# Performance work log

Measured on AMD Instinct MI355X. Metric: run time of the kernel, lower is better.

Reference implementation:

```python
import jax, jax.numpy as jnp
import numpy as np

B, S, V, D, G, H, L, K = 32, 256, 100000, 128, 128, 256, 32, 3
ALPHA = 0.5


def lstm_pass(x, mask, W, U, b, reverse):
    # x: (B,S,I), mask: (B,S) bool. PyTorch gate order i,f,g,o.
    Bh = x.shape[0]
    Hd = U.shape[0]
    h0 = jnp.zeros((Bh, Hd), x.dtype)
    c0 = jnp.zeros((Bh, Hd), x.dtype)

    def step(carry, inp):
        h, c = carry
        xt, mt = inp
        g = xt @ W + h @ U + b
        i, f, gg, o = jnp.split(g, 4, axis=-1)
        i = jax.nn.sigmoid(i)
        f = jax.nn.sigmoid(f)
        gg = jnp.tanh(gg)
        o = jax.nn.sigmoid(o)
        cn = f * c + i * gg
        hn = o * jnp.tanh(cn)
        m = mt[:, None]
        h = jnp.where(m, hn, h)
        c = jnp.where(m, cn, c)
        return (h, c), h * m.astype(h.dtype)

    _, hs = jax.lax.scan(step, (h0, c0), (x.transpose(1, 0, 2), mask.T), reverse=reverse)
    return hs.transpose(1, 0, 2)  # (B,S,Hd), zero at padded steps (like pad_packed)


def setup_inputs() -> dict:
    key = jax.random.key(0)
    ks = jax.random.split(key, 24)
    word_inputs = jax.random.randint(ks[0], (B, S), 0, V)
    lens = jnp.sort(jax.random.randint(ks[1], (B,), S // 2, S + 1))[::-1]
    mask = (jnp.arange(S)[None, :] < lens[:, None])
    idx_inputs = jax.random.randint(ks[2], (B, S), 0, V)
    char_inputs = jax.random.randint(ks[3], (B * S, 4), 0, 100)
    char_seq_lengths = jnp.ones((B * S,), jnp.int64 if jax.config.jax_enable_x64 else jnp.int32)
    char_seq_recover = jnp.arange(B * S)
    s = lambda k, sh, sc: jax.random.normal(k, sh, jnp.float32) * sc
    I = D + G
    inp = {
        'word_inputs': word_inputs,
        'word_seq_lengths': lens,
        'char_inputs': char_inputs,
        'char_seq_lengths': char_seq_lengths,
        'char_seq_recover': char_seq_recover,
        'mask': mask,
        'idx_inputs': idx_inputs,
        'word_embedding': s(ks[4], (V, D), 0.1),
        'label_embedding': s(ks[5], (L, D), 0.1),
        'sent_W': s(ks[6], (D, G), 1.0 / np.sqrt(D)),
        'sent_b': jnp.zeros((G,), jnp.float32),
        'conv_W': s(ks[7], (L, L, K), 1.0 / np.sqrt(L * K)),
        'conv_b': jnp.zeros((L,), jnp.float32),
        'lstm_Wf': s(ks[8], (I, 4 * H // 2), 1.0 / np.sqrt(I)),
        'lstm_Uf': s(ks[9], (H // 2, 4 * H // 2), 1.0 / np.sqrt(H // 2)),
        'lstm_bf': jnp.zeros((4 * H // 2,), jnp.float32),
        'lstm_Wb': s(ks[10], (I, 4 * H // 2), 1.0 / np.sqrt(I)),
        'lstm_Ub': s(ks[11], (H // 2, 4 * H // 2), 1.0 / np.sqrt(H // 2)),
        'lstm_bb': jnp.zeros((4 * H // 2,), jnp.float32),
        'tag_W': s(ks[12], (H, L), 1.0 / np.sqrt(H)),
        'tag_b': jnp.zeros((L,), jnp.float32),
        'mem_W': s(ks[13], (H, L), 1.0 / np.sqrt(H)),
        'mem_b': jnp.zeros((L,), jnp.float32),
        'mem_bank': s(ks[14], (V, H), 0.1),
    }
    return inp


def reference(word_inputs, word_seq_lengths, char_inputs, char_seq_lengths, char_seq_recover,
              mask, idx_inputs, word_embedding, label_embedding, sent_W, sent_b,
              conv_W, conv_b, lstm_Wf, lstm_Uf, lstm_bf, lstm_Wb, lstm_Ub, lstm_bb,
              tag_W, tag_b, mem_W, mem_b, mem_bank):
    maskf = mask.astype(jnp.float32)
    # ---- WordRep: embeddings + label cosine similarity ----
    we = word_embedding[word_inputs]  # (B,S,D) gather
    wn = we / (jnp.linalg.norm(we, axis=-1, keepdims=True) + 1e-8)
    ln = label_embedding / (jnp.linalg.norm(label_embedding, axis=-1, keepdims=True) + 1e-8)
    label_embs = jnp.einsum('bsd,ld->bsl', wn, ln)  # (B,S,L)
    # ---- SentenceRep (projection stand-in) + label attention pooling ----
    sent_hidden = jnp.tanh(we @ sent_W + sent_b)  # (B,S,G)
    lf = jax.lax.conv_general_dilated(
        label_embs.transpose(0, 2, 1), conv_W, (1,), [(K // 2, K // 2)],
        dimension_numbers=('NCH', 'OIH', 'NCH')) + conv_b[None, :, None]
    lf = jax.nn.relu(lf).transpose(0, 2, 1)  # (B,S,L)
    lm = lf.max(axis=-1)  # (B,S)
    # partial (masked) softmax, exactly as in the torch code
    e = jnp.exp(lm) * maskf
    attn = e / e.sum(axis=1, keepdims=True)
    sent_rep = jnp.einsum('bs,bsg->bg', attn, sent_hidden)[:, None, :]  # bmm
    sent_rep = jnp.broadcast_to(sent_rep, (B, S, G))  # repeat over seq
    # ---- BiLSTM over concat(word, sentence) ----
    wr = jnp.concatenate([we, sent_rep], axis=-1)  # (B,S,D+G)
    hf = lstm_pass(wr, mask, lstm_Wf, lstm_Uf, lstm_bf, False)
    hb = lstm_pass(wr, mask, lstm_Wb, lstm_Ub, lstm_bb, True)
    feat = jnp.concatenate([hf, hb], axis=-1)  # (B,S,H)
    outputs = feat @ tag_W + tag_b  # (B,S,L)
    # ---- MemoryBank: gather keyed by word id, zero padded positions ----
    doc_h = mem_bank[word_inputs] * maskf[..., None]  # (B,S,H) irregular gather
    doc_rep = doc_h @ mem_W + mem_b  # mem2tag
    # bank update (side effect in torch; computed functionally, not returned)
    new_bank = mem_bank.at[idx_inputs.reshape(-1)].set(
        (feat * maskf[..., None]).reshape(-1, H))
    del new_bank
    return outputs * (1.0 - ALPHA) + doc_rep * ALPHA
```

## Files before the change

kernel.cpp:

```cpp
#include <hip/hip_runtime.h>
#include <hip/hip_bf16.h>

#define BB 32
#define SS 256
#define DD 128
#define GG 128
#define NG 512
#define LL 32
#define LOG2E 1.4426950408889634f

typedef unsigned short u16;
typedef __attribute__((ext_vector_type(8))) short short8;
typedef __attribute__((ext_vector_type(4))) float f32x4;

__device__ __forceinline__ float bf2f(u16 u){ return __uint_as_float(((unsigned)u)<<16); }
__device__ __forceinline__ u16 f2bf(float f){
    unsigned x = __float_as_uint(f);
    unsigned r = x + 0x7fffu + ((x>>16)&1u);
    return (u16)(r>>16);
}
__device__ __forceinline__ float tanh_f(float x){ float e=__expf(2.0f*x); return 1.0f - 2.0f/(e+1.0f); }

__device__ __forceinline__ float exp2_f(float x){
#if __has_builtin(__builtin_amdgcn_exp2f)
    return __builtin_amdgcn_exp2f(x);
#elif __has_builtin(__builtin_amdgcn_expf)
    return __builtin_amdgcn_expf(x);
#else
    return __expf(x * 0.6931471805599453f);
#endif
}
__device__ __forceinline__ float rcp_f(float x){
#if __has_builtin(__builtin_amdgcn_rcpf)
    return __builtin_amdgcn_rcpf(x);
#else
    return 1.0f / x;
#endif
}

struct PJobs { const void* src[21]; int n[21]; int p0[21]; int p1[21]; int type[21]; };

__global__ void kprep(PJobs jb, const void* __restrict__ wemb, int* __restrict__ flags,
                      float* __restrict__ can,
                      u16* __restrict__ WcatT, u16* __restrict__ tagWT, u16* __restrict__ memWT){
    int t = threadIdx.x;
    __shared__ int cw[4];
    __shared__ int sflag;
    {
        u16 v = ((const u16*)wemb)[2*t];
        int e = (v>>7)&0xFF;
        int c = (e>=0x90)?1:0;
        #pragma unroll
        for (int mk=32; mk>0; mk>>=1) c += __shfl_xor(c, mk);
        if ((t&63)==0) cw[t>>6] = c;
        __syncthreads();
        if (t==0) sflag = (cw[0]+cw[1]+cw[2]+cw[3] >= 32) ? 1 : 0;
        __syncthreads();
    }
    int f = sflag;
    if (blockIdx.x==0 && blockIdx.y==0 && t==0) flags[0] = f;

    int id = blockIdx.y;
    int i = blockIdx.x*256 + t;
    if (i >= jb.n[id]) return;
    const void* src = jb.src[id];
    int p0 = jb.p0[id];
    int ty = jb.type[id];
    if (ty == 0){
        float v = f ? ((const float*)src)[i] : bf2f(((const u16*)src)[i]);
        can[p0 + i] = v;
    } else if (ty == 1){
        int c = i>>7, k = i&127;
        float v = f ? ((const float*)src)[k*jb.p1[id] + c] : bf2f(((const u16*)src)[k*jb.p1[id] + c]);
        WcatT[(size_t)(p0 + c)*128 + k] = f2bf(v);
    } else if (ty == 2){
        int l = i&31, k = i>>5;
        float v = f ? ((const float*)src)[k*32 + l] : bf2f(((const u16*)src)[k*32 + l]);
        (p0 ? memWT : tagWT)[l*256 + k] = f2bf(v);
    } else {
        int row = i>>7, col = i&127;
        float v = f ? ((const float*)src)[i] : bf2f(((const u16*)src)[i]);
        float sq = v*v;
        #pragma unroll
        for (int mk=32; mk>0; mk>>=1) sq += __shfl_xor(sq, mk);
        __shared__ float r4[4];
        if ((t&63)==0) r4[t>>6] = sq;
        __syncthreads();
        int half = t>>7;
        float tot = r4[half*2] + r4[half*2+1];
        float inv = 1.0f/(sqrtf(tot) + 1e-8f);
        WcatT[(size_t)(1152+row)*128 + col] = f2bf(v*inv);
        WcatT[(size_t)(1184+row)*128 + col] = 0;
    }
}

__global__ void k1_token(const int* __restrict__ wid, const void* __restrict__ wemb,
                         const int* __restrict__ flags,
                         u16* __restrict__ weC, float* __restrict__ invn){
    int blk = blockIdx.x;
    int t = threadIdx.x;
    int idx = wid[blk];
    float wv = flags[0] ? ((const float*)wemb)[(size_t)idx*DD + t]
                        : bf2f(((const u16*)wemb)[(size_t)idx*DD + t]);
    int b = blk>>8, s = blk&255;
    int m = s*BB + b;
    weC[(size_t)m*DD + t] = f2bf(wv);
    float sq = wv*wv;
    #pragma unroll
    for (int mk=32; mk>0; mk>>=1) sq += __shfl_xor(sq, mk);
    __shared__ float red2[2];
    if ((t&63)==0) red2[t>>6] = sq;
    __syncthreads();
    if (t==0) invn[m] = 1.0f/(sqrtf(red2[0]+red2[1]) + 1e-8f);
}

__global__ __launch_bounds__(256) void kgemm(const u16* __restrict__ weC,
                      const u16* __restrict__ WcatT,
                      const float* __restrict__ invn, const float* __restrict__ sentBc,
                      float* __restrict__ gpre4, float* __restrict__ sent_h,
                      float* __restrict__ lab_e){
    int mt = blockIdx.x;
    int nb = blockIdx.y;
    int t = threadIdx.x;
    int w4 = t>>6, l = t&63, li = l&15, lg = l>>4;
    int mbase = mt*64 + w4*16;
    int n0 = nb*64;
    short8 af[4];
    #pragma unroll
    for (int ks=0;ks<4;ks++)
        af[ks] = *(const short8*)&weC[(size_t)(mbase + li)*128 + ks*32 + lg*8];
    f32x4 acc[4];
    #pragma unroll
    for (int nt=0;nt<4;nt++){
        short8 bf[4];
        #pragma unroll
        for (int ks=0;ks<4;ks++)
            bf[ks] = *(const short8*)&WcatT[(size_t)(n0 + nt*16 + li)*128 + ks*32 + lg*8];
        f32x4 a; a[0]=0.f; a[1]=0.f; a[2]=0.f; a[3]=0.f;
        #pragma unroll
        for (int ks=0;ks<4;ks++)
            a = __builtin_amdgcn_mfma_f32_16x16x32_bf16(af[ks], bf[ks], a, 0,0,0);
        acc[nt] = a;
    }
    int mrow = mbase + lg*4;
    #pragma unroll
    for (int nt=0;nt<4;nt++){
        int n = n0 + nt*16 + li;
        if (n < 1024){
            int dir = n>>9, n2 = n&511;
            int q = n2>>7, cc = n2&127, w5 = cc>>4, li5 = cc&15;
            float sc = (q==2) ? 2.0f*LOG2E : LOG2E;
            #pragma unroll
            for (int r=0;r<4;r++){
                int m = mrow + r;
                int b = m&31, s = m>>5;
                int bg = b>>2, rb = b&3;
                gpre4[((size_t)((dir*8+bg)*256 + s)*8 + w5)*256 + (rb*16 + li5)*4 + q] = acc[nt][r]*sc;
            }
        } else if (n < 1152){
            int c = n - 1024;
            float bb = sentBc[c];
            #pragma unroll
            for (int r=0;r<4;r++){
                int m = mrow + r;
                int b = m&31, s = m>>5;
                sent_h[((size_t)(b*256+s))*128 + c] = tanh_f(acc[nt][r] + bb);
            }
        } else if (n < 1184){
            int c = n - 1152;
            #pragma unroll
            for (int r=0;r<4;r++){
                int m = mrow + r;
                int b = m&31, s = m>>5;
                lab_e[((size_t)(b*256+s))*32 + c] = acc[nt][r] * invn[m];
            }
        }
    }
}

__global__ __launch_bounds__(256) void k2_conv(const float* __restrict__ lab_e,
                        const float* __restrict__ convWc, const float* __restrict__ convBc,
                        const int* __restrict__ lens, float* __restrict__ e_ws){
    int b = blockIdx.x, stile = blockIdx.y, t = threadIdx.x;
    int sl = t>>3, oq = t&7;
    int s = stile*32 + sl;
    __shared__ float le_s[34*33];
    __shared__ float wle[LL*LL*3];
    __shared__ float wb[LL];
    int s0 = stile*32;
    for (int i=t; i<34*32; i+=256){
        int row = i>>5, col = i&31;
        int sg = s0 - 1 + row;
        le_s[row*33 + col] = (sg>=0 && sg<SS) ? lab_e[(size_t)b*SS*LL + sg*LL + col] : 0.f;
    }
    for (int i=t; i<LL*LL*3; i+=256) wle[i] = convWc[i];
    if (t < LL) wb[t] = convBc[t];
    __syncthreads();
    float lm = 0.f;
    #pragma unroll
    for (int op=0; op<4; op++){
        int o = oq*4 + op;
        float a0 = wb[o], a1 = 0.f, a2 = 0.f;
        #pragma unroll
        for (int i=0;i<LL;i++){
            a0 = fmaf(le_s[(sl+0)*33+i], wle[o*96 + i*3    ], a0);
            a1 = fmaf(le_s[(sl+1)*33+i], wle[o*96 + i*3 + 1], a1);
            a2 = fmaf(le_s[(sl+2)*33+i], wle[o*96 + i*3 + 2], a2);
        }
        lm = fmaxf(lm, fmaxf(a0+a1+a2, 0.f));
    }
    #pragma unroll
    for (int mk=1; mk<8; mk<<=1) lm = fmaxf(lm, __shfl_xor(lm, mk));
    if (oq == 0) e_ws[b*SS + s] = (s < lens[b]) ? __expf(lm) : 0.f;
}

__global__ void k3a_attn(const float* __restrict__ e_ws, const float* __restrict__ sent_h,
                         float* __restrict__ srp, float* __restrict__ esum_p){
    int b = blockIdx.x, st = blockIdx.y, t = threadIdx.x;
    int col = t&127, sh = t>>7;
    __shared__ float es[32];
    __shared__ float red[2][GG];
    if (t < 32) es[t] = e_ws[b*SS + st*32 + t];
    __syncthreads();
    int sb = st*32 + sh*16;
    float a0 = 0.f, a1 = 0.f;
    #pragma unroll
    for (int s2=0; s2<16; s2+=2){
        a0 = fmaf(es[sh*16+s2],   sent_h[((size_t)b*SS + sb+s2)*GG + col], a0);
        a1 = fmaf(es[sh*16+s2+1], sent_h[((size_t)b*SS + sb+s2+1)*GG + col], a1);
    }
    red[sh][col] = a0+a1;
    __syncthreads();
    if (t < GG) srp[((size_t)b*8 + st)*GG + t] = red[0][t] + red[1][t];
    if (t < 32){
        float e = es[t];
        #pragma unroll
        for (int mk=16; mk>0; mk>>=1) e += __shfl_xor(e, mk);
        if (t==0) esum_p[b*8 + st] = e;
    }
}

__global__ void k3b_cpart(const float* __restrict__ srp, const float* __restrict__ esum_p,
                          const float* __restrict__ Wfc, const float* __restrict__ Wbc,
                          const float* __restrict__ bfc, const float* __restrict__ bbc,
                          float* __restrict__ cpart){
    int chunk = blockIdx.x, b = blockIdx.y, t = threadIdx.x;
    __shared__ float srs[GG];
    if (t < GG){
        float a = 0.f;
        #pragma unroll
        for (int st=0; st<8; st++) a += srp[((size_t)b*8 + st)*GG + t];
        float es = 0.f;
        #pragma unroll
        for (int st=0; st<8; st++) es += esum_p[b*8 + st];
        srs[t] = a * (1.0f/es);
    }
    __syncthreads();
    int ng = chunk*256 + t;
    int dir = ng>>9, n = ng&511;
    const float* W = dir ? Wbc : Wfc;
    float c0 = (dir ? bbc : bfc)[n], c1 = 0.f;
    for (int g=0; g<GG; g+=2){
        c0 = fmaf(srs[g],   W[(size_t)(DD+g)*NG + n], c0);
        c1 = fmaf(srs[g+1], W[(size_t)(DD+g+1)*NG + n], c1);
    }
    cpart[((size_t)dir*NG + n)*BB + b] = c0+c1;
}

__global__ __launch_bounds__(512) void k5_lstm(const float* __restrict__ gpre4,
                       const float* __restrict__ Ufc, const float* __restrict__ Ubc,
                       const float* __restrict__ cpart,
                       const int* __restrict__ lens, float* __restrict__ feat){
    int dir = blockIdx.x>>3, bg = blockIdx.x&7;
    int t = threadIdx.x;
    int w = t>>6, l = t&63, lg = l>>4, li = l&15;
    int j = w*16 + li;
    int b = bg*4 + lg;
    const float* Uc = dir ? Ubc : Ufc;

    short8 bfr[4][4];
    #pragma unroll
    for (int q=0;q<4;q++){
        float sc = (q==2) ? 2.0f*LOG2E : LOG2E;
        #pragma unroll
        for (int ks=0;ks<4;ks++){
            int n = q*128 + j;
            short8 v;
            #pragma unroll
            for (int jj=0;jj<8;jj++)
                v[jj] = (short)f2bf(Uc[(size_t)(ks*32 + lg*8 + jj)*NG + n] * sc);
            bfr[q][ks] = v;
        }
    }
    float cpr[4];
    #pragma unroll
    for (int q=0;q<4;q++)
        cpr[q] = cpart[((size_t)(dir*NG + q*128 + j))*BB + b] * ((q==2) ? 2.0f*LOG2E : LOG2E);
    int len1 = lens[b];

    __shared__ u16 Hhi[2][16*128];
    for (int i=t; i<2*2048; i+=512) ((u16*)Hhi)[i] = 0;

    bool rdp = ((li & 3) == 0);
    int roff[4];
    #pragma unroll
    for (int ks=0;ks<4;ks++)
        roff[ks] = (li*256 + ((ks*64 + lg*16) ^ ((li&7)<<4))) >> 1;
    int woff;
    { int row = lg*4; woff = (row*256 + ((2*j) ^ ((row&7)<<4))) >> 1; }

    short8 ah[4];
    #pragma unroll
    for (int ks=0;ks<4;ks++){
        #pragma unroll
        for (int jj=0;jj<8;jj++) ah[ks][jj] = 0;
    }

    float c = 0.f, h = 0.f;
    int sgn = dir ? -1 : 1;
    int s0 = dir ? (SS-1) : 0;
    const float* gl = gpre4 + ((size_t)(dir*8 + bg)*256 + s0)*2048 + w*256 + l*4;
    ptrdiff_t gstep = (ptrdiff_t)sgn * 2048;

    f32x4 gA = *(const f32x4*)gl;
    f32x4 gB = *(const f32x4*)(gl + gstep);
    const float* glp = gl + 2*gstep;

    float* fb = feat + ((size_t)b*SS + s0)*256 + dir*128 + j;
    ptrdiff_t fstep = (ptrdiff_t)sgn * 256;

    int s = s0;
    __syncthreads();

#define K5_STEP(P, G)                                                          \
    {                                                                          \
        if (rdp){                                                              \
            ah[0] = *(const short8*)&Hhi[P][roff[0]];                          \
            ah[1] = *(const short8*)&Hhi[P][roff[1]];                          \
            ah[2] = *(const short8*)&Hhi[P][roff[2]];                          \
            ah[3] = *(const short8*)&Hhi[P][roff[3]];                          \
        }                                                                      \
        f32x4 ac[4];                                                           \
        _Pragma("unroll")                                                      \
        for (int q=0;q<4;q++){ f32x4 z; z[0]=G[q]+cpr[q]; z[1]=0.f; z[2]=0.f; z[3]=0.f; ac[q]=z; } \
        if (tt2 + 2 < SS){ G = *(const f32x4*)glp; glp += gstep; }             \
        _Pragma("unroll")                                                      \
        for (int ks=0;ks<4;ks++){                                              \
            _Pragma("unroll")                                                  \
            for (int q=0;q<4;q++)                                              \
                ac[q] = __builtin_amdgcn_mfma_f32_16x16x32_bf16(ah[ks], bfr[q][ks], ac[q], 0,0,0); \
        }                                                                      \
        float si = rcp_f(1.0f + exp2_f(-ac[0][0]));                            \
        float sf = rcp_f(1.0f + exp2_f(-ac[1][0]));                            \
        float tg = 1.0f - 2.0f*rcp_f(exp2_f(ac[2][0]) + 1.0f);                 \
        float so = rcp_f(1.0f + exp2_f(-ac[3][0]));                            \
        float cn = sf*c + si*tg;                                               \
        float th = 1.0f - 2.0f*rcp_f(exp2_f(cn*(2.0f*LOG2E)) + 1.0f);          \
        float hn = so*th;                                                      \
        if (s < 128){ c = cn; h = hn; fb[0] = hn; }                            \
        else { bool mm = (s < len1); c = mm?cn:c; h = mm?hn:h; fb[0] = mm?hn:0.f; } \
        Hhi[P^1][woff] = f2bf(h);                                              \
        asm volatile("s_waitcnt lgkmcnt(0)" ::: "memory");                     \
        __builtin_amdgcn_sched_barrier(0);                                     \
        __builtin_amdgcn_s_barrier();                                          \
        __builtin_amdgcn_sched_barrier(0);                                     \
        s += sgn; fb += fstep;                                                 \
    }

    for (int tt=0; tt<SS; tt+=2){
        { int tt2 = tt;   K5_STEP(0, gA) }
        { int tt2 = tt+1; K5_STEP(1, gB) }
    }
#undef K5_STEP
}

__global__ void k6_final(const float* __restrict__ feat, const int* __restrict__ wid,
                         const int* __restrict__ lens,
                         const u16* __restrict__ tagWT, const float* __restrict__ tagBc,
                         const u16* __restrict__ memWT, const float* __restrict__ memBc,
                         const void* __restrict__ bank, const int* __restrict__ flags,
                         void* __restrict__ out){
    int t = threadIdx.x;
    int tok = blockIdx.x*8 + (t>>5);
    int lcol = t&31;
    int b = tok>>8, s = tok&255;
    int f32m = flags[0];
    int idx = wid[tok];
    bool m = s < lens[b];
    const float* fr = feat + (size_t)tok*256;
    float a0 = tagBc[lcol], a1=0.f, a2=0.f, a3=0.f;
    #pragma unroll 4
    for (int cc=0; cc<32; cc++){
        short8 tw = *(const short8*)&tagWT[lcol*256 + cc*8];
        a0 = fmaf(fr[cc*8+0], bf2f((u16)tw[0]), a0);
        a1 = fmaf(fr[cc*8+1], bf2f((u16)tw[1]), a1);
        a2 = fmaf(fr[cc*8+2], bf2f((u16)tw[2]), a2);
        a3 = fmaf(fr[cc*8+3], bf2f((u16)tw[3]), a3);
        a0 = fmaf(fr[cc*8+4], bf2f((u16)tw[4]), a0);
        a1 = fmaf(fr[cc*8+5], bf2f((u16)tw[5]), a1);
        a2 = fmaf(fr[cc*8+6], bf2f((u16)tw[6]), a2);
        a3 = fmaf(fr[cc*8+7], bf2f((u16)tw[7]), a3);
    }
    float r1 = (a0+a1)+(a2+a3);
    float b0 = memBc[lcol], b1=0.f, b2=0.f, b3=0.f;
    if (m){
        if (f32m){
            const float* br = (const float*)bank + (size_t)idx*256;
            #pragma unroll 4
            for (int cc=0; cc<32; cc++){
                short8 tw = *(const short8*)&memWT[lcol*256 + cc*8];
                b0 = fmaf(br[cc*8+0], bf2f((u16)tw[0]), b0);
                b1 = fmaf(br[cc*8+1], bf2f((u16)tw[1]), b1);
                b2 = fmaf(br[cc*8+2], bf2f((u16)tw[2]), b2);
                b3 = fmaf(br[cc*8+3], bf2f((u16)tw[3]), b3);
                b0 = fmaf(br[cc*8+4], bf2f((u16)tw[4]), b0);
                b1 = fmaf(br[cc*8+5], bf2f((u16)tw[5]), b1);
                b2 = fmaf(br[cc*8+6], bf2f((u16)tw[6]), b2);
                b3 = fmaf(br[cc*8+7], bf2f((u16)tw[7]), b3);
            }
        } else {
            const u16* br = (const u16*)bank + (size_t)idx*256;
            #pragma unroll 4
            for (int cc=0; cc<32; cc++){
                short8 tw = *(const short8*)&memWT[lcol*256 + cc*8];
                short8 bv = *(const short8*)&br[cc*8];
                b0 = fmaf(bf2f((u16)bv[0]), bf2f((u16)tw[0]), b0);
                b1 = fmaf(bf2f((u16)bv[1]), bf2f((u16)tw[1]), b1);
                b2 = fmaf(bf2f((u16)bv[2]), bf2f((u16)tw[2]), b2);
                b3 = fmaf(bf2f((u16)bv[3]), bf2f((u16)tw[3]), b3);
                b0 = fmaf(bf2f((u16)bv[4]), bf2f((u16)tw[4]), b0);
                b1 = fmaf(bf2f((u16)bv[5]), bf2f((u16)tw[5]), b1);
                b2 = fmaf(bf2f((u16)bv[6]), bf2f((u16)tw[6]), b2);
                b3 = fmaf(bf2f((u16)bv[7]), bf2f((u16)tw[7]), b3);
            }
        }
    }
    float r2 = (b0+b1)+(b2+b3);
    float res = 0.5f*r1 + 0.5f*r2;
    if (f32m) ((float*)out)[(size_t)tok*LL + lcol] = res;
    else      ((u16*)out)[(size_t)tok*LL + lcol]   = f2bf(res);
}

extern "C" void kernel_launch(void* const* d_in, const int* in_sizes, int n_in,
                              void* d_out, int out_size, void* d_ws, size_t ws_size,
                              hipStream_t stream){
    const int* wid  = (const int*)d_in[0];
    const int* lens = (const int*)d_in[1];

    char* ws = (char*)d_ws;
    int*   flags  = (int*)  (ws + 0);
    float* can    = (float*)(ws + 1024);
    u16*   WcatT  = (u16*)  (ws + 1900544);
    u16*   tagWT  = (u16*)  (ws + 2211840);
    u16*   memWT  = (u16*)  (ws + 2228224);
    float* invn   = (float*)(ws + 2244608);
    float* cpart  = (float*)(ws + 2277376);
    float* e_ws   = (float*)(ws + 2408448);
    float* srp    = (float*)(ws + 2441216);
    float* esum_p = (float*)(ws + 2572288);
    u16*   weC    = (u16*)  (ws + 4194304);
    float* lab_e  = (float*)(ws + 8388608);
    float* sent_h = (float*)(ws + 9437184);
    float* gpre4  = (float*)(ws + 16777216);
    float* feat   = (float*)(ws + 50331648);

    float* sentBc = can + 20480;
    float* convWc = can + 20608;
    float* convBc = can + 23680;
    float* Wfc    = can + 23712;
    float* Wbc    = can + 154784;
    float* bfc    = can + 285856;
    float* bbc    = can + 286368;
    float* Ufc    = can + 286880;
    float* Ubc    = can + 352416;
    float* tagBc  = can + 426144;
    float* memBc  = can + 434368;

    static const int cn_n[15]   = {4096,16384,128,3072,32,131072,131072,512,512,65536,65536,8192,32,8192,32};
    static const int cn_src[15] = {8,9,10,11,12,13,16,15,18,14,17,19,20,21,22};
    PJobs jb;
    {
        int off = 0;
        for (int i=0;i<15;i++){
            jb.src[i]=d_in[cn_src[i]]; jb.n[i]=cn_n[i]; jb.p0[i]=off; jb.p1[i]=0; jb.type[i]=0;
            off+=cn_n[i];
        }
        jb.src[15]=d_in[13]; jb.n[15]=65536; jb.p0[15]=0;    jb.p1[15]=512; jb.type[15]=1;
        jb.src[16]=d_in[16]; jb.n[16]=65536; jb.p0[16]=512;  jb.p1[16]=512; jb.type[16]=1;
        jb.src[17]=d_in[9];  jb.n[17]=16384; jb.p0[17]=1024; jb.p1[17]=128; jb.type[17]=1;
        jb.src[18]=d_in[19]; jb.n[18]=8192;  jb.p0[18]=0;    jb.p1[18]=0;   jb.type[18]=2;
        jb.src[19]=d_in[21]; jb.n[19]=8192;  jb.p0[19]=1;    jb.p1[19]=0;   jb.type[19]=2;
        jb.src[20]=d_in[8];  jb.n[20]=4096;  jb.p0[20]=0;    jb.p1[20]=0;   jb.type[20]=3;
    }

    kprep  <<<dim3(512,21), 256, 0, stream>>>(jb, d_in[7], flags, can, WcatT, tagWT, memWT);
    k1_token<<<8192, 128, 0, stream>>>(wid, d_in[7], flags, weC, invn);
    kgemm  <<<dim3(128,19), 256, 0, stream>>>(weC, WcatT, invn, sentBc, gpre4, sent_h, lab_e);
    k2_conv<<<dim3(32,8), 256, 0, stream>>>(lab_e, convWc, convBc, lens, e_ws);
    k3a_attn<<<dim3(32,8), 256, 0, stream>>>(e_ws, sent_h, srp, esum_p);
    k3b_cpart<<<dim3(4,32), 256, 0, stream>>>(srp, esum_p, Wfc, Wbc, bfc, bbc, cpart);
    k5_lstm<<<16, 512, 0, stream>>>(gpre4, Ufc, Ubc, cpart, lens, feat);
    k6_final<<<1024, 256, 0, stream>>>(feat, wid, lens, tagWT, tagBc, memWT, memBc,
                                       d_in[23], flags, d_out);
}
```

Measured before the change: 241.2 us.

## Permute LSTM input weights for vector gate stores and fuse conv with attention

The LSTM input-projection weights are now permuted during prep so that each GEMM tile's four 16-column subtiles hold the i,f,g,o gates for the same hidden units. The GEMM epilogue can then write gate preactivations as contiguous float4 stores instead of scattered scalar writes. The conv/max kernel and the attention-partial kernel are merged into one, so the exp scores stay in shared memory and one launch and one global round trip are removed. The LSTM step also reuses a persistent accumulator array instead of re-zeroing per step. The risk is that the index permutation must match the gpre4 layout exactly.

```diff
diff --git a/kernel.cpp b/kernel.cpp
--- a/kernel.cpp
+++ b/kernel.cpp
@@ -77,7 +77,7 @@
         int l = i&31, k = i>>5;
         float v = f ? ((const float*)src)[k*32 + l] : bf2f(((const u16*)src)[k*32 + l]);
         (p0 ? memWT : tagWT)[l*256 + k] = f2bf(v);
-    } else {
+    } else if (ty == 3){
         int row = i>>7, col = i&127;
         float v = f ? ((const float*)src)[i] : bf2f(((const u16*)src)[i]);
         float sq = v*v;
@@ -91,6 +91,11 @@
         float inv = 1.0f/(sqrtf(tot) + 1e-8f);
         WcatT[(size_t)(1152+row)*128 + col] = f2bf(v*inv);
         WcatT[(size_t)(1184+row)*128 + col] = 0;
+    } else {
+        int c = i>>7, k = i&127;
+        float v = f ? ((const float*)src)[k*512 + c] : bf2f(((const u16*)src)[k*512 + c]);
+        int q = c>>7, rem = c&127, w5 = rem>>4, li = rem&15;
+        WcatT[(size_t)(p0 + w5*64 + q*16 + li)*128 + k] = f2bf(v);
     }
 }
 
@@ -142,51 +147,60 @@
             a = __builtin_amdgcn_mfma_f32_16x16x32_bf16(af[ks], bf[ks], a, 0,0,0);
         acc[nt] = a;
     }
-    int mrow = mbase + lg*4;
-    #pragma unroll
-    for (int nt=0;nt<4;nt++){
-        int n = n0 + nt*16 + li;
-        if (n < 1024){
-            int dir = n>>9, n2 = n&511;
-            int q = n2>>7, cc = n2&127, w5 = cc>>4, li5 = cc&15;
-            float sc = (q==2) ? 2.0f*LOG2E : LOG2E;
-            #pragma unroll
-            for (int r=0;r<4;r++){
-                int m = mrow + r;
-                int b = m&31, s = m>>5;
-                int bg = b>>2, rb = b&3;
-                gpre4[((size_t)((dir*8+bg)*256 + s)*8 + w5)*256 + (rb*16 + li5)*4 + q] = acc[nt][r]*sc;
-            }
-        } else if (n < 1152){
-            int c = n - 1024;
-            float bb = sentBc[c];
-            #pragma unroll
-            for (int r=0;r<4;r++){
-                int m = mrow + r;
-                int b = m&31, s = m>>5;
-                sent_h[((size_t)(b*256+s))*128 + c] = tanh_f(acc[nt][r] + bb);
-            }
-        } else if (n < 1184){
-            int c = n - 1152;
-            #pragma unroll
-            for (int r=0;r<4;r++){
-                int m = mrow + r;
-                int b = m&31, s = m>>5;
-                lab_e[((size_t)(b*256+s))*32 + c] = acc[nt][r] * invn[m];
+    if (nb < 16){
+        int dir = nb>>3, w5 = nb&7;
+        int s = mt*2 + (w4>>1);
+        int bg = (w4&1)*4 + lg;
+        float* gp = gpre4 + ((((size_t)(dir*8+bg)*256 + s)*8 + w5)*256);
+        #pragma unroll
+        for (int r=0;r<4;r++){
+            f32x4 v;
+            v[0] = acc[0][r]*LOG2E;
+            v[1] = acc[1][r]*LOG2E;
+            v[2] = acc[2][r]*(2.0f*LOG2E);
+            v[3] = acc[3][r]*LOG2E;
+            *(f32x4*)&gp[(r*16 + li)*4] = v;
+        }
+    } else {
+        int mrow = mbase + lg*4;
+        #pragma unroll
+        for (int nt=0;nt<4;nt++){
+            int n = n0 + nt*16 + li;
+            if (n < 1152){
+                int c = n - 1024;
+                float bb = sentBc[c];
+                #pragma unroll
+                for (int r=0;r<4;r++){
+                    int m = mrow + r;
+                    int b = m&31, s = m>>5;
+                    sent_h[((size_t)(b*256+s))*128 + c] = tanh_f(acc[nt][r] + bb);
+                }
+            } else if (n < 1184){
+                int c = n - 1152;
+                #pragma unroll
+                for (int r=0;r<4;r++){
+                    int m = mrow + r;
+                    int b = m&31, s = m>>5;
+                    lab_e[((size_t)(b*256+s))*32 + c] = acc[nt][r] * invn[m];
+                }
             }
         }
     }
 }
 
-__global__ __launch_bounds__(256) void k2_conv(const float* __restrict__ lab_e,
+__global__ __launch_bounds__(256) void k23p(const float* __restrict__ lab_e,
                         const float* __restrict__ convWc, const float* __restrict__ convBc,
-                        const int* __restrict__ lens, float* __restrict__ e_ws){
+                        const float* __restrict__ sent_h,
+                        const int* __restrict__ lens,
+                        float* __restrict__ srp, float* __restrict__ esum_p){
     int b = blockIdx.x, stile = blockIdx.y, t = threadIdx.x;
     int sl = t>>3, oq = t&7;
     int s = stile*32 + sl;
     __shared__ float le_s[34*33];
     __shared__ float wle[LL*LL*3];
     __shared__ float wb[LL];
+    __shared__ float es[32];
+    __shared__ float red[2][GG];
     int s0 = stile*32;
     for (int i=t; i<34*32; i+=256){
         int row = i>>5, col = i&31;
@@ -211,19 +225,11 @@
     }
     #pragma unroll
     for (int mk=1; mk<8; mk<<=1) lm = fmaxf(lm, __shfl_xor(lm, mk));
-    if (oq == 0) e_ws[b*SS + s] = (s < lens[b]) ? __expf(lm) : 0.f;
-}
-
-__global__ void k3a_attn(const float* __restrict__ e_ws, const float* __restrict__ sent_h,
-                         float* __restrict__ srp, float* __restrict__ esum_p){
-    int b = blockIdx.x, st = blockIdx.y, t = threadIdx.x;
+    if (oq == 0) es[sl] = (s < lens[b]) ? __expf(lm) : 0.f;
+    __syncthreads();
     int col = t&127, sh = t>>7;
-    __shared__ float es[32];
-    __shared__ float red[2][GG];
-    if (t < 32) es[t] = e_ws[b*SS + st*32 + t];
-    __syncthreads();
-    int sb = st*32 + sh*16;
     float a0 = 0.f, a1 = 0.f;
+    int sb = s0 + sh*16;
     #pragma unroll
     for (int s2=0; s2<16; s2+=2){
         a0 = fmaf(es[sh*16+s2],   sent_h[((size_t)b*SS + sb+s2)*GG + col], a0);
@@ -231,12 +237,12 @@
     }
     red[sh][col] = a0+a1;
     __syncthreads();
-    if (t < GG) srp[((size_t)b*8 + st)*GG + t] = red[0][t] + red[1][t];
+    if (t < GG) srp[((size_t)b*8 + stile)*GG + t] = red[0][t] + red[1][t];
     if (t < 32){
         float e = es[t];
         #pragma unroll
         for (int mk=16; mk>0; mk>>=1) e += __shfl_xor(e, mk);
-        if (t==0) esum_p[b*8 + st] = e;
+        if (t==0) esum_p[b*8 + stile] = e;
     }
 }
 
@@ -315,6 +321,9 @@
         #pragma unroll
         for (int jj=0;jj<8;jj++) ah[ks][jj] = 0;
     }
+    f32x4 acv[4];
+    #pragma unroll
+    for (int q=0;q<4;q++){ acv[q][0]=0.f; acv[q][1]=0.f; acv[q][2]=0.f; acv[q][3]=0.f; }
 
     float c = 0.f, h = 0.f;
     int sgn = dir ? -1 : 1;
@@ -340,20 +349,21 @@
             ah[2] = *(const short8*)&Hhi[P][roff[2]];                          \
             ah[3] = *(const short8*)&Hhi[P][roff[3]];                          \
         }                                                                      \
-        f32x4 ac[4];                                                           \
-        _Pragma("unroll")                                                      \
-        for (int q=0;q<4;q++){ f32x4 z; z[0]=G[q]+cpr[q]; z[1]=0.f; z[2]=0.f; z[3]=0.f; ac[q]=z; } \
+        acv[0][0] = G[0]+cpr[0];                                               \
+        acv[1][0] = G[1]+cpr[1];                                               \
+        acv[2][0] = G[2]+cpr[2];                                               \
+        acv[3][0] = G[3]+cpr[3];                                               \
         if (tt2 + 2 < SS){ G = *(const f32x4*)glp; glp += gstep; }             \
         _Pragma("unroll")                                                      \
         for (int ks=0;ks<4;ks++){                                              \
             _Pragma("unroll")                                                  \
             for (int q=0;q<4;q++)                                              \
-                ac[q] = __builtin_amdgcn_mfma_f32_16x16x32_bf16(ah[ks], bfr[q][ks], ac[q], 0,0,0); \
+                acv[q] = __builtin_amdgcn_mfma_f32_16x16x32_bf16(ah[ks], bfr[q][ks], acv[q], 0,0,0); \
         }                                                                      \
-        float si = rcp_f(1.0f + exp2_f(-ac[0][0]));                            \
-        float sf = rcp_f(1.0f + exp2_f(-ac[1][0]));                            \
-        float tg = 1.0f - 2.0f*rcp_f(exp2_f(ac[2][0]) + 1.0f);                 \
-        float so = rcp_f(1.0f + exp2_f(-ac[3][0]));                            \
+        float si = rcp_f(1.0f + exp2_f(-acv[0][0]));                           \
+        float sf = rcp_f(1.0f + exp2_f(-acv[1][0]));                           \
+        float tg = 1.0f - 2.0f*rcp_f(exp2_f(acv[2][0]) + 1.0f);                \
+        float so = rcp_f(1.0f + exp2_f(-acv[3][0]));                           \
         float cn = sf*c + si*tg;                                               \
         float th = 1.0f - 2.0f*rcp_f(exp2_f(cn*(2.0f*LOG2E)) + 1.0f);          \
         float hn = so*th;                                                      \
@@ -455,7 +465,6 @@
     u16*   memWT  = (u16*)  (ws + 2228224);
     float* invn   = (float*)(ws + 2244608);
     float* cpart  = (float*)(ws + 2277376);
-    float* e_ws   = (float*)(ws + 2408448);
     float* srp    = (float*)(ws + 2441216);
     float* esum_p = (float*)(ws + 2572288);
     u16*   weC    = (u16*)  (ws + 4194304);
@@ -485,8 +494,8 @@
             jb.src[i]=d_in[cn_src[i]]; jb.n[i]=cn_n[i]; jb.p0[i]=off; jb.p1[i]=0; jb.type[i]=0;
             off+=cn_n[i];
         }
-        jb.src[15]=d_in[13]; jb.n[15]=65536; jb.p0[15]=0;    jb.p1[15]=512; jb.type[15]=1;
-        jb.src[16]=d_in[16]; jb.n[16]=65536; jb.p0[16]=512;  jb.p1[16]=512; jb.type[16]=1;
+        jb.src[15]=d_in[13]; jb.n[15]=65536; jb.p0[15]=0;    jb.p1[15]=512; jb.type[15]=4;
+        jb.src[16]=d_in[16]; jb.n[16]=65536; jb.p0[16]=512;  jb.p1[16]=512; jb.type[16]=4;
         jb.src[17]=d_in[9];  jb.n[17]=16384; jb.p0[17]=1024; jb.p1[17]=128; jb.type[17]=1;
         jb.src[18]=d_in[19]; jb.n[18]=8192;  jb.p0[18]=0;    jb.p1[18]=0;   jb.type[18]=2;
         jb.src[19]=d_in[21]; jb.n[19]=8192;  jb.p0[19]=1;    jb.p1[19]=0;   jb.type[19]=2;
@@ -496,8 +505,7 @@
     kprep  <<<dim3(512,21), 256, 0, stream>>>(jb, d_in[7], flags, can, WcatT, tagWT, memWT);
     k1_token<<<8192, 128, 0, stream>>>(wid, d_in[7], flags, weC, invn);
     kgemm  <<<dim3(128,19), 256, 0, stream>>>(weC, WcatT, invn, sentBc, gpre4, sent_h, lab_e);
-    k2_conv<<<dim3(32,8), 256, 0, stream>>>(lab_e, convWc, convBc, lens, e_ws);
-    k3a_attn<<<dim3(32,8), 256, 0, stream>>>(e_ws, sent_h, srp, esum_p);
+    k23p   <<<dim3(32,8), 256, 0, stream>>>(lab_e, convWc, convBc, sent_h, lens, srp, esum_p);
     k3b_cpart<<<dim3(4,32), 256, 0, stream>>>(srp, esum_p, Wfc, Wbc, bfc, bbc, cpart);
     k5_lstm<<<16, 512, 0, stream>>>(gpre4, Ufc, Ubc, cpart, lens, feat);
     k6_final<<<1024, 256, 0, stream>>>(feat, wid, lens, tagWT, tagBc, memWT, memBc,
```

Result: faster. 223.4 us (-7.4%).
